# Performance work log

Hardware: AMD Instinct MI355X
Metric: run time of the kernel (lower is better)

The kernel has to match this reference:

```python
import jax, jax.numpy as jnp
import numpy as np

N_MOL, N_ATOM, DEG = 32, 128, 32
N = N_MOL * N_ATOM          # 4096 real atoms (no blanks)
P = N * DEG                 # 131072 pairs
N_SENS = 20
SOFT_MIN, SOFT_MAX, HARD_MAX = 0.7, 5.0, 7.5
N_IN, N_OUT, N_HIST = 2, 3, 3
NF1 = 20                    # hipnn1 n_features
NF0 = 2 * NF1               # hipnn0 n_features (doubled in __init__)
NG = 4 * NF1                # gate logits width of InteractLayer W
N_ATOM_LAYERS = 3
NIN0 = 2 + N_HIST           # one-hot over {1,8} + x_h channels


def setup_inputs():
    rng = np.random.default_rng(0)
    species = 1 + 7 * rng.integers(0, 2, size=(N_MOL, N_ATOM))  # values in {1,8}, all nonblank
    base = np.repeat(np.arange(N), DEG)
    local = base % N_ATOM
    neigh = (local + 1 + rng.integers(0, N_ATOM - 1, size=P)) % N_ATOM  # neighbor != self
    pair_second = (base // N_ATOM) * N_ATOM + neigh                     # same-molecule pairs
    key = jax.random.key(0)
    ks = jax.random.split(key, 20)
    g = lambda i, shape, s=0.1: jax.random.normal(ks[i], shape, dtype=jnp.float32) * s
    return {
        "species": jnp.asarray(species, jnp.int32),
        "coordinates": jax.random.uniform(ks[0], (N_MOL, N_ATOM, 3), jnp.float32, 0.0, 6.0),
        "x_h": g(1, (N_MOL, N_ATOM, N_HIST)),
        "x_raw": g(2, (N_MOL, N_ATOM, N_IN)),
        "pair_first": jnp.asarray(base, jnp.int32),
        "pair_second": jnp.asarray(pair_second, jnp.int32),
        "h0_int_w": g(3, (N_SENS, NIN0, NF0)),
        "h0_self_w": g(4, (NIN0, NF0)),
        "h0_self_b": g(5, (NF0,)),
        "h0_aw": g(6, (N_ATOM_LAYERS, NF0, NF0)),
        "h0_ab": g(7, (N_ATOM_LAYERS, NF0)),
        "h1_int_w": g(8, (N_SENS, 1, NF1)),
        "h1_self_w": g(9, (1, NF1)),
        "h1_self_b": g(10, (NF1,)),
        "h1_aw": g(11, (N_ATOM_LAYERS, NF1, NF1)),
        "h1_ab": g(12, (N_ATOM_LAYERS, NF1)),
        "W_int_w": g(13, (N_SENS, NF0, NG)),
        "W_self_w": g(14, (NF0, NG)),
        "W_self_b": g(15, (NG,)),
        "pw0": g(16, (NIN0, 1)),
        "pw1": g(17, (NF1, 1)),
        "pb1": g(18, (1,)),
    }


def _sensitivity(d):
    # inverse-distance gaussian sensitivities with smooth hard cutoff
    mu = jnp.linspace(1.0 / SOFT_MAX, 1.0 / SOFT_MIN, N_SENS)
    sigma = (1.0 / SOFT_MIN - 1.0 / SOFT_MAX) / N_SENS
    sense = jnp.exp(-0.5 * jnp.square((1.0 / d[:, None] - mu) / sigma))
    cut = jnp.where(d < HARD_MAX, jnp.square(jnp.cos(jnp.pi * d / (2.0 * HARD_MAX))), 0.0)
    return sense * cut[:, None]                                     # (P, n_sens)


def _interact(x, sense, pf, ps, int_w, self_w, self_b):
    # gather neighbor features, weight by sensitivities, scatter-add to center atom
    msg = sense[:, :, None] * x[ps][:, None, :]                     # (P, ns, fin)
    env = jax.ops.segment_sum(msg, pf, num_segments=N)              # (N, ns, fin)
    ns, fin, fout = int_w.shape
    return env.reshape(N, ns * fin) @ int_w.reshape(ns * fin, fout) + x @ self_w + self_b


def _hipnn(x, sense, pf, ps, int_w, self_w, self_b, aw, ab):
    y = jax.nn.softplus(_interact(x, sense, pf, ps, int_w, self_w, self_b))
    for i in range(aw.shape[0]):
        y = jax.nn.softplus(y @ aw[i] + ab[i])
    return x, y   # (input features, final block features)


def _forward(coordinates, x_h, x_raw,
             h0_int_w, h0_self_w, h0_self_b, h0_aw, h0_ab,
             h1_int_w, h1_self_w, h1_self_b, h1_aw, h1_ab,
             W_int_w, W_self_w, W_self_b, pw0, pw1, pb1,
             species, pair_first, pair_second):
    enc = (species.reshape(-1)[:, None] == jnp.array([1, 8])).astype(jnp.float32)  # OneHotSpecies
    coord = coordinates.reshape(-1, 3)
    diff = coord[pair_first] - coord[pair_second]
    d = jnp.sqrt(jnp.sum(diff * diff, axis=-1) + 1e-12)
    sense = _sensitivity(d)
    ind_f = jnp.concatenate([enc, x_h.reshape(N, N_HIST)], axis=1)  # (N, 5)
    f0_in, f0_out = _hipnn(ind_f, sense, pair_first, pair_second,
                           h0_int_w, h0_self_w, h0_self_b, h0_aw, h0_ab)
    c_t, h_t = f0_out[:, : NF0 // 2], f0_out[:, NF0 // 2:]

    def onestep(x_in, h_t, c_t):
        x_t = _hipnn(x_in, sense, pair_first, pair_second,
                     h1_int_w, h1_self_w, h1_self_b, h1_aw, h1_ab)[1]
        tmp = _interact(jnp.concatenate([x_t, h_t], axis=-1), sense,
                        pair_first, pair_second, W_int_w, W_self_w, W_self_b)
        tmp = tmp.reshape(N, NF1, 4)
        o_t = jax.nn.sigmoid(tmp[..., 3])
        c_t = jax.nn.sigmoid(tmp[..., 1]) * c_t + jax.nn.sigmoid(tmp[..., 0]) * jnp.tanh(tmp[..., 2])
        h_t = o_t * jnp.tanh(c_t)
        return o_t, h_t, c_t

    xr = x_raw.reshape(N, N_IN)
    o_t = None
    for t in range(N_IN):
        o_t, h_t, c_t = onestep(xr[:, t:t + 1], h_t, c_t)
    x0 = f0_in @ pw0 + o_t @ pw1 + pb1                              # PredictAtom
    outs = []
    for t in range(N_OUT):
        o_t, h_t, c_t = onestep(x0, h_t, c_t)
        x0 = f0_in @ pw0 + o_t @ pw1 + pb1
        outs.append(x0)
    return jnp.concatenate(outs, axis=-1)                           # (N, n_out)


def reference(species, coordinates, x_h, x_raw, pair_first, pair_second,
              h0_int_w, h0_self_w, h0_self_b, h0_aw, h0_ab,
              h1_int_w, h1_self_w, h1_self_b, h1_aw, h1_ab,
              W_int_w, W_self_w, W_self_b, pw0, pw1, pb1):
    return _forward(coordinates, x_h, x_raw,
                    h0_int_w, h0_self_w, h0_self_b, h0_aw, h0_ab,
                    h1_int_w, h1_self_w, h1_self_b, h1_aw, h1_ab,
                    W_int_w, W_self_w, W_self_b, pw0, pw1, pb1,
                    species, pair_first, pair_second)
```

## Files before the change

kernel.cpp:

```cpp
#include <hip/hip_runtime.h>
#include <hip/hip_bf16.h>


#define DEG 32
#define NA 4096
#define NP 131072

typedef __hip_bfloat16 bf16;
typedef __attribute__((ext_vector_type(8))) short short8v;
typedef __attribute__((ext_vector_type(4))) float f32x4;

#define Z0F 16.27906976744186f
#define DZ  1.0526315789473684f

__device__ __forceinline__ float frcp(float x){ return __builtin_amdgcn_rcpf(x); }
__device__ __forceinline__ float sigmoid_f(float x){ return frcp(1.f + __expf(-x)); }
__device__ __forceinline__ float tanh_f(float x){ return 1.f - 2.f*frcp(__expf(2.f*x)+1.f); }
__device__ __forceinline__ float softplus_f(float x){ return fmaxf(x,0.f) + __logf(1.f + __expf(-fabsf(x))); }
__device__ __forceinline__ unsigned bf16pack(float lo, float hi){
  unsigned ul = __float_as_uint(lo), uh = __float_as_uint(hi);
  unsigned rl = (ul + 0x7fffu + ((ul>>16)&1u)) >> 16;
  unsigned rh = (uh + 0x7fffu + ((uh>>16)&1u)) & 0xffff0000u;
  return rl | rh;
}
__device__ __forceinline__ unsigned short b16u(float v){
  unsigned u = __float_as_uint(v);
  return (unsigned short)((u + 0x7fffu + ((u>>16)&1u)) >> 16);
}
union UU { unsigned u[4]; short8v v; };
union U4 { uint4 q; short8v v; unsigned u[4]; };

__device__ __forceinline__ void wr_tile(unsigned* er, f32x4 D, int M, int N,
                                        int lg, int lr, int l){
  #pragma unroll
  for(int r=0;r<4;r++){
    float vd = D[r];
    float pr = __shfl_xor(vd, 1);
    int s = M*16 + lg*4 + r, f = N*16 + lr;
    if(!(l&1) && s<20 && f<40) er[s*20 + (f>>1)] = bf16pack(vd, pr);
  }
}

__global__ __launch_bounds__(256) void k_prep(
    const int* __restrict__ pf, const int* __restrict__ ps,
    const int* __restrict__ species,
    const float* __restrict__ coord, const float* __restrict__ xh,
    const float* __restrict__ pw0, const float* __restrict__ pb1,
    const float* __restrict__ Wint, const float* __restrict__ Wself,
    unsigned short* __restrict__ svA, unsigned* __restrict__ svB,
    unsigned* __restrict__ Amf,
    bf16* __restrict__ Wmf, float* __restrict__ indf, float* __restrict__ proj0)
{
  int b = blockIdx.x, t = threadIdx.x;
  if (b < 512){
    int p = b*256 + t;
    int i = pf[p], j = ps[p];
    float dx = coord[i*3+0]-coord[j*3+0];
    float dy = coord[i*3+1]-coord[j*3+1];
    float dz = coord[i*3+2]-coord[j*3+2];
    float d = sqrtf(dx*dx+dy*dy+dz*dz + 1e-12f);
    float cu = 0.f;
    if (d < 7.5f){ float c = __cosf(d * 0.20943951023931953f); cu = c*c; }
    float z0 = (1.f/d - 0.2f)*Z0F;
    int atom = p>>5, k = p&31;
    float sv[20], svn[20];
    #pragma unroll
    for(int s=0;s<20;s++){
      float z = z0 - (float)s*DZ;
      sv[s] = cu*__expf(-0.5f*z*z);
    }
    #pragma unroll
    for(int s=0;s<20;s++) svn[s] = __shfl_down(sv[s], 1);
    #pragma unroll
    for(int s=0;s<20;s++) svA[atom*640 + s*32 + k] = b16u(sv[s]);
    #pragma unroll
    for(int s2=0;s2<10;s2++) svB[atom*320 + k*10 + s2] = bf16pack(sv[2*s2], sv[2*s2+1]);
    if (!(k&1)){
      int lg = k>>3, q = (k>>1)&3;
      #pragma unroll
      for(int s=0;s<20;s++){
        int lr = s&15, fr = s>>4;
        Amf[atom*512 + (lg*16+lr)*8 + fr*4 + q] = bf16pack(sv[s], svn[s]);
      }
    } else {
      int idx = k>>1;
      int lg2 = idx>>2, q2 = idx&3;
      #pragma unroll
      for(int j2=0;j2<12;j2++){
        int lr = 4+j2;
        Amf[atom*512 + (lg2*16+lr)*8 + 4 + q2] = 0u;
      }
    }
  } else if (b < 782){
    int tid = (b-512)*256 + t;
    if (tid < 69120){
      int j = tid & 7, l = (tid>>3) & 63, gt = (tid>>9)%5, slab = tid/2560;
      int k = slab*32 + ((l>>4)<<3) + j;
      int g = gt*16 + (l&15);
      float v = 0.f;
      if (k < 800)      v = Wint[k*80+g];
      else if (k < 840) v = Wself[(k-800)*80+g];
      Wmf[tid] = __float2bfloat16(v);
    }
  } else {
    int tid = (b-782)*256 + t;
    if (tid < NA){
      int sp = species[tid];
      float f0 = (sp==1)?1.f:0.f, f1 = (sp==8)?1.f:0.f;
      float f2=xh[tid*3+0], f3=xh[tid*3+1], f4=xh[tid*3+2];
      indf[tid*5+0]=f0; indf[tid*5+1]=f1; indf[tid*5+2]=f2;
      indf[tid*5+3]=f3; indf[tid*5+4]=f4;
      proj0[tid] = pb1[0] + f0*pw0[0] + f1*pw0[1] + f2*pw0[2]
                 + f3*pw0[3] + f4*pw0[4];
    }
  }
}

#define F_SVT  0
#define F_INDF 10432
#define F_ENV0 11072
#define F_Y0A  12672
#define F_Y0B  13312
#define F_NB   13952
#define F_SMEM 14080
__device__ void f0_body(float* smem, int t, int mol, int sib,
    const int* __restrict__ ps, const unsigned* __restrict__ svB,
    const float* __restrict__ indf_g,
    const float* __restrict__ h0_iw, const float* __restrict__ h0_sw,
    const float* __restrict__ h0_sb, const float* __restrict__ h0_aw,
    const float* __restrict__ h0_ab,
    float* __restrict__ c_g, unsigned* __restrict__ h_p)
{
  const int nbase = mol*128;
  const int abase = nbase + sib*16;
  float* svt  = smem + F_SVT;
  float* indf = smem + F_INDF;
  float* env0 = smem + F_ENV0;
  float* y0a  = smem + F_Y0A;
  float* y0b  = smem + F_Y0B;
  unsigned char* nb8 = (unsigned char*)(smem + F_NB);

  for(int i=t;i<5120;i+=512){
    int a=i/320, q=i%320, k=q/10, s2=q%10;
    unsigned v = svB[(abase+a)*320 + q];
    float* dst = svt + a*652 + k*20 + s2*2;
    dst[0] = __uint_as_float(v<<16);
    dst[1] = __uint_as_float(v & 0xffff0000u);
  }
  for(int i=t;i<640;i+=512) indf[i] = indf_g[nbase*5 + i];
  if (t < 512) nb8[t] = (unsigned char)(ps[abase*DEG + t] - nbase);
  __syncthreads();

  for(int task=t; task<1600; task+=512){
    int a = task/100, e = task%100, s = e/5, f = e%5;
    const float* svr = svt + a*652;
    const unsigned char* nbr = nb8 + a*32;
    float acc = 0.f;
    for(int k=0;k<32;k++) acc += svr[k*20+s]*indf[nbr[k]*5+f];
    env0[a*100+e] = acc;
  }
  __syncthreads();
  for(int task=t; task<640; task+=512){
    int a=task/40, o=task%40, row=(sib*16)+a;
    float acc = h0_sb[o];
    #pragma unroll
    for(int f=0;f<5;f++) acc += indf[row*5+f]*h0_sw[f*40+o];
    for(int e=0;e<100;e++) acc += env0[a*100+e]*h0_iw[e*40+o];
    y0a[a*40+o] = softplus_f(acc);
  }
  __syncthreads();
  float* cur = y0a; float* nxt = y0b;
  for(int l=0;l<3;l++){
    for(int task=t; task<640; task+=512){
      int a=task/40, o=task%40;
      float acc = h0_ab[l*40+o];
      for(int f=0;f<40;f++) acc += cur[a*40+f]*h0_aw[l*1600+f*40+o];
      nxt[a*40+o] = softplus_f(acc);
    }
    __syncthreads();
    float* tswap=cur; cur=nxt; nxt=tswap;
  }
  if (t < 320){ int a=t/20,u=t%20; c_g[(abase+a)*20+u] = cur[a*40+u]; }
  if (t < 160){ int a=t/10,p=t%10;
    h_p[NA*10 + (abase+a)*10+p] = bf16pack(cur[a*40+20+2*p], cur[a*40+21+2*p]); }
}

#define X_XIN 0
#define X_NB  128
#define X_WTS 256
#define X_EV1 1956
#define X_YA  2276
#define X_YB  2596
__device__ void xt_body(float* smem, int t, int mol, int sib,
    const int* __restrict__ ps, const unsigned short* __restrict__ svA,
    const float* __restrict__ xraw, const float* __restrict__ x0g,
    int use_raw, int col,
    const float* __restrict__ h1_iw, const float* __restrict__ h1_sw,
    const float* __restrict__ h1_sb, const float* __restrict__ h1_aw,
    const float* __restrict__ h1_ab,
    unsigned* __restrict__ xt_p)
{
  const int nbase = mol*128;
  const int abase = nbase + sib*16;
  float* xin = smem + X_XIN;
  unsigned char* nb8 = (unsigned char*)(smem + X_NB);
  float* wts = smem + X_WTS;
  float* ev1 = smem + X_EV1;
  float* yA  = smem + X_YA;
  float* yB  = smem + X_YB;

  if (t < 128) xin[t] = use_raw ? xraw[(nbase+t)*2+col] : x0g[nbase+t];
  if (t < 512) nb8[t] = (unsigned char)(ps[abase*DEG+t] - nbase);
  for(int i=t;i<1700;i+=512){
    float v;
    if(i<400){ int o=i/20,s=i%20; v=h1_iw[s*20+o]; }
    else if(i<420) v=h1_sw[i-400];
    else if(i<440) v=h1_sb[i-420];
    else if(i<1640){ int q=i-440,L=q/400,rem=q%400,o=rem/20,f=rem%20; v=h1_aw[L*400+f*20+o]; }
    else v=h1_ab[i-1640];
    wts[i]=v;
  }
  __syncthreads();

  if (t < 320){
    int a=t/20, s=t%20;
    const uint4* sp4 = (const uint4*)(svA + (abase+a)*640 + s*32);
    const unsigned char* nbr = nb8 + a*32;
    float acc = 0.f;
    #pragma unroll
    for(int c4=0;c4<4;c4++){
      uint4 w = sp4[c4];
      unsigned wu[4] = {w.x,w.y,w.z,w.w};
      #pragma unroll
      for(int j=0;j<4;j++){
        float flo = __uint_as_float(wu[j]<<16);
        float fhi = __uint_as_float(wu[j] & 0xffff0000u);
        int k = c4*8 + 2*j;
        acc += flo*xin[nbr[k]] + fhi*xin[nbr[k+1]];
      }
    }
    ev1[t] = acc;
  }
  __syncthreads();
  if (t < 320){
    int a=t/20, o=t%20;
    float acc = wts[420+o] + xin[sib*16+a]*wts[400+o];
    const float* e = ev1 + a*20; const float* w = wts + o*20;
    #pragma unroll
    for(int s=0;s<20;s++) acc += e[s]*w[s];
    yA[t] = softplus_f(acc);
  }
  __syncthreads();
  #pragma unroll
  for(int L=0;L<2;L++){
    const float* src = (L==0)? yA : yB;
    float* dst       = (L==0)? yB : yA;
    if (t < 320){
      int a=t/20, o=t%20;
      float acc = wts[1640+L*20+o];
      const float* sr = src + a*20; const float* w = wts + 440 + L*400 + o*20;
      #pragma unroll
      for(int f=0;f<20;f++) acc += sr[f]*w[f];
      dst[t] = softplus_f(acc);
    }
    __syncthreads();
  }
  if (t < 160){
    int a=t/10, p=t%10, o0=2*p, o1=o0+1;
    const float* e = yA + a*20;
    float a0 = wts[1680+o0], a1 = wts[1680+o1];
    const float* wA = wts + 1240 + o0*20;
    const float* wB = wA + 20;
    #pragma unroll
    for(int f=0;f<20;f++){ a0 += e[f]*wA[f]; a1 += e[f]*wB[f]; }
    xt_p[(abase+a)*10+p] = bf16pack(softplus_f(a0), softplus_f(a1));
  }
}

__global__ __launch_bounds__(512) void k_fx(
    const int* __restrict__ ps, const unsigned* __restrict__ svB,
    const unsigned short* __restrict__ svA,
    const float* __restrict__ indf_g, const float* __restrict__ xraw,
    const float* __restrict__ h0_iw, const float* __restrict__ h0_sw,
    const float* __restrict__ h0_sb, const float* __restrict__ h0_aw,
    const float* __restrict__ h0_ab,
    const float* __restrict__ h1_iw, const float* __restrict__ h1_sw,
    const float* __restrict__ h1_sb, const float* __restrict__ h1_aw,
    const float* __restrict__ h1_ab,
    float* __restrict__ c_g, unsigned* __restrict__ h_p,
    unsigned* __restrict__ xt_p0, unsigned* __restrict__ xt_p1)
{
  __shared__ float smem[F_SMEM];
  const int t = threadIdx.x;
  const int sel = blockIdx.x >> 8;
  const int blk = blockIdx.x & 255;
  const int mol = blk & 31, sib = blk >> 5;
  if (sel == 0)
    f0_body(smem, t, mol, sib, ps, svB, indf_g,
            h0_iw,h0_sw,h0_sb,h0_aw,h0_ab, c_g, h_p);
  else
    xt_body(smem, t, mol, sib, ps, svA, xraw, (const float*)0, 1, sel-1,
            h1_iw,h1_sw,h1_sb,h1_aw,h1_ab, (sel==1)? xt_p0 : xt_p1);
}

__global__ __launch_bounds__(512) void k_xt(
    const int* __restrict__ ps, const unsigned short* __restrict__ svA,
    const float* __restrict__ xraw, const float* __restrict__ x0g,
    const float* __restrict__ h1_iw, const float* __restrict__ h1_sw,
    const float* __restrict__ h1_sb, const float* __restrict__ h1_aw,
    const float* __restrict__ h1_ab,
    unsigned* __restrict__ xt_p)
{
  __shared__ float smem[2916];
  const int t = threadIdx.x;
  const int mol = blockIdx.x & 31, sib = blockIdx.x >> 5;
  xt_body(smem, t, mol, sib, ps, svA, xraw, x0g, 0, 0,
          h1_iw,h1_sw,h1_sb,h1_aw,h1_ab, xt_p);
}

#define E_XHP 0
#define E_NB  2688
#define E_PRJ 2752
#define E_PW1 2768
#define E_ER  2792
#define E_TMP (E_ER+6976)
#define E_RED (E_TMP+1280)
#define E_HT  (E_RED+160)
#define E_SMEM (E_HT+160)
__global__ __launch_bounds__(512) void k_env(
    const int* __restrict__ ps, const unsigned* __restrict__ Amf,
    const unsigned* __restrict__ xt_p, const unsigned* __restrict__ h_p,
    int rpar, int wpar,
    const bf16* __restrict__ Wmf, const float* __restrict__ Wb,
    const float* __restrict__ pw1, const float* __restrict__ proj0,
    float* __restrict__ c_g, unsigned* __restrict__ h_po,
    float* __restrict__ x0g, float* __restrict__ outp, int out_col)
{
  __shared__ float smem[E_SMEM];
  const int t = threadIdx.x;
  const int mol = blockIdx.x & 31, sib = blockIdx.x >> 5;
  const int nbase = mol*128;
  const int abase = nbase + sib*8;
  unsigned* xhp = (unsigned*)(smem + E_XHP);
  unsigned char* nb8 = (unsigned char*)(smem + E_NB);
  float* prj  = smem + E_PRJ;
  float* pw1s = smem + E_PW1;
  unsigned* er = (unsigned*)(smem + E_ER);

  for(int i=t;i<1280;i+=512){
    int r=i/10, p=i%10;
    xhp[r*21+p]    = xt_p[(nbase+r)*10+p];
    xhp[r*21+10+p] = h_p[rpar*NA*10 + (nbase+r)*10+p];
  }
  if (t < 256) nb8[t] = (unsigned char)(ps[abase*DEG + t] - nbase);
  if (t < 8)  prj[t] = proj0[abase+t];
  if (t < 20) pw1s[t] = pw1[t];
  __syncthreads();

  {
    const int wv = t>>6, l = t&63, lg = (t>>4)&3, lr = t&15;
    f32x4 z4 = {0.f,0.f,0.f,0.f};
    int a = wv;
    int atom_g = abase + a;
    const U4* ap = (const U4*)(Amf + (unsigned)atom_g*512u + (unsigned)l*8u);
    U4 A0 = ap[0], A1 = ap[1];
    const unsigned* nbw = (const unsigned*)(nb8 + a*32 + lg*8);
    unsigned nw0=nbw[0], nw1=nbw[1];
    int nl[8];
    #pragma unroll
    for(int j2=0;j2<4;j2++){ nl[j2]=(nw0>>(8*j2))&255; nl[4+j2]=(nw1>>(8*j2))&255; }
    f32x4 d00,d01,d02,d10,d11,d12;
    {
      UU B; int f=lr; unsigned sh=(f&1)<<4;
      #pragma unroll
      for(int q=0;q<4;q++){
        unsigned wlo = xhp[nl[2*q]*21 + (f>>1)];
        unsigned whi = xhp[nl[2*q+1]*21 + (f>>1)];
        B.u[q] = ((wlo>>sh)&0xffffu) | (((whi>>sh)&0xffffu)<<16);
      }
      d00=__builtin_amdgcn_mfma_f32_16x16x32_bf16(A0.v,B.v,z4,0,0,0);
      d10=__builtin_amdgcn_mfma_f32_16x16x32_bf16(A1.v,B.v,z4,0,0,0);
    }
    {
      UU B; int f=16+lr; unsigned sh=(f&1)<<4;
      #pragma unroll
      for(int q=0;q<4;q++){
        unsigned wlo = xhp[nl[2*q]*21 + (f>>1)];
        unsigned whi = xhp[nl[2*q+1]*21 + (f>>1)];
        B.u[q] = ((wlo>>sh)&0xffffu) | (((whi>>sh)&0xffffu)<<16);
      }
      d01=__builtin_amdgcn_mfma_f32_16x16x32_bf16(A0.v,B.v,z4,0,0,0);
      d11=__builtin_amdgcn_mfma_f32_16x16x32_bf16(A1.v,B.v,z4,0,0,0);
    }
    {
      UU B; int f=32+lr; unsigned sh=(f&1)<<4; int val=(f<40);
      #pragma unroll
      for(int q=0;q<4;q++){
        if (val){
          unsigned wlo = xhp[nl[2*q]*21 + (f>>1)];
          unsigned whi = xhp[nl[2*q+1]*21 + (f>>1)];
          B.u[q] = ((wlo>>sh)&0xffffu) | (((whi>>sh)&0xffffu)<<16);
        } else B.u[q] = 0u;
      }
      d02=__builtin_amdgcn_mfma_f32_16x16x32_bf16(A0.v,B.v,z4,0,0,0);
      d12=__builtin_amdgcn_mfma_f32_16x16x32_bf16(A1.v,B.v,z4,0,0,0);
    }
    unsigned* era = er + a*436;
    wr_tile(era,d00,0,0,lg,lr,l); wr_tile(era,d01,0,1,lg,lr,l);
    wr_tile(era,d02,0,2,lg,lr,l); wr_tile(era,d10,1,0,lg,lr,l);
    wr_tile(era,d11,1,1,lg,lr,l); wr_tile(era,d12,1,2,lg,lr,l);
  }
  if (t < 160){ int a=t/20, f2=t%20; er[a*436+400+f2] = xhp[(sib*8+a)*21+f2]; }
  if (t < 256) er[(t>>4)*436 + 420 + (t&15)] = 0u;
  __syncthreads();

  float* tmp_s = smem + E_TMP;
  if (t < 320){
    int wv = t >> 6, l = t & 63;
    f32x4 cacc = {0.f,0.f,0.f,0.f};
    const unsigned* abase_p = er + (l & 15)*436 + ((l>>4)<<2);
    const short8v* bptr = (const short8v*)Wmf + (wv*64 + l);
    #pragma unroll 3
    for(int slab=0; slab<27; ++slab){
      short8v av = *(const short8v*)(abase_p + slab*16);
      short8v bv = bptr[slab*320];
      cacc = __builtin_amdgcn_mfma_f32_16x16x32_bf16(av, bv, cacc, 0,0,0);
    }
    int g = wv*16 + (l & 15);
    float wb = Wb[g];
    int r0 = (l>>4)*4;
    #pragma unroll
    for(int r=0;r<4;r++) tmp_s[(r0+r)*80 + g] = cacc[r] + wb;
  }
  __syncthreads();

  float* red = smem + E_RED;
  float* ht  = smem + E_HT;
  if (t < 160){
    int a=t/20, u=t%20;
    float4 tv = *(const float4*)(tmp_s + a*80 + u*4);
    float cold = c_g[(abase+a)*20+u];
    float cnew = sigmoid_f(tv.y)*cold + sigmoid_f(tv.x)*tanh_f(tv.z);
    float og   = sigmoid_f(tv.w);
    c_g[(abase+a)*20+u] = cnew;
    ht[a*20+u]  = og*tanh_f(cnew);
    red[a*20+u] = og*pw1s[u];
  }
  __syncthreads();
  if (t < 80){
    int a=t/10, p=t%10;
    h_po[wpar*NA*10 + (abase+a)*10+p] = bf16pack(ht[a*20+2*p], ht[a*20+2*p+1]);
  }
  if (t < 8){
    float accx = prj[t];
    #pragma unroll
    for(int u=0;u<20;u++) accx += red[t*20+u];
    x0g[abase+t] = accx;
    if (out_col >= 0) outp[(abase+t)*3+out_col] = accx;
  }
}

extern "C" void kernel_launch(void* const* d_in, const int* in_sizes, int n_in,
                              void* d_out, int out_size, void* d_ws, size_t ws_size,
                              hipStream_t stream)
{
  const int*   species = (const int*)  d_in[0];
  const float* coord   = (const float*)d_in[1];
  const float* xh      = (const float*)d_in[2];
  const float* xraw    = (const float*)d_in[3];
  const int*   pf      = (const int*)  d_in[4];
  const int*   ps      = (const int*)  d_in[5];
  const float* h0_intw = (const float*)d_in[6];
  const float* h0_sw   = (const float*)d_in[7];
  const float* h0_sb   = (const float*)d_in[8];
  const float* h0_aw   = (const float*)d_in[9];
  const float* h0_ab   = (const float*)d_in[10];
  const float* h1_intw = (const float*)d_in[11];
  const float* h1_sw   = (const float*)d_in[12];
  const float* h1_sb   = (const float*)d_in[13];
  const float* h1_aw   = (const float*)d_in[14];
  const float* h1_ab   = (const float*)d_in[15];
  const float* W_intw  = (const float*)d_in[16];
  const float* W_sw    = (const float*)d_in[17];
  const float* W_sb    = (const float*)d_in[18];
  const float* pw0     = (const float*)d_in[19];
  const float* pw1     = (const float*)d_in[20];
  const float* pb1     = (const float*)d_in[21];
  float* outp = (float*)d_out;

  float* w = (float*)d_ws;
  unsigned short* svA = (unsigned short*)w;  w += NA*320;
  unsigned* svB = (unsigned*)w;              w += NA*320;
  unsigned* Amf = (unsigned*)w;              w += NA*512;
  bf16* Wmf = (bf16*)w;                      w += 34560;
  float* indf = w;                           w += NA*5;
  float* proj0 = w;                          w += NA;
  unsigned* xt_pA = (unsigned*)w;            w += NA*10;
  unsigned* xt_pB = (unsigned*)w;            w += NA*10;
  unsigned* h_p = (unsigned*)w;              w += 2*NA*10;
  float* x0g = w;                            w += NA;
  float* c_g = w;                            w += NA*20;

  k_prep<<<800,256,0,stream>>>(pf,ps,species,coord,xh,pw0,pb1,W_intw,W_sw,
                               svA,svB,Amf,Wmf,indf,proj0);
  k_fx<<<768,512,0,stream>>>(ps,svB,svA,indf,xraw,
                             h0_intw,h0_sw,h0_sb,h0_aw,h0_ab,
                             h1_intw,h1_sw,h1_sb,h1_aw,h1_ab,
                             c_g,h_p,xt_pA,xt_pB);
  for(int step=0; step<5; ++step){
    int rpar = (step+1)&1, wpar = step&1;
    int out_col = (step>=2)? (step-2) : -1;
    unsigned* xtp = (step&1)? xt_pB : xt_pA;
    if (step >= 2)
      k_xt<<<256,512,0,stream>>>(ps,svA,xraw,x0g,
                                 h1_intw,h1_sw,h1_sb,h1_aw,h1_ab, xtp);
    k_env<<<512,512,0,stream>>>(ps,Amf,xtp,h_p,rpar,wpar,
                                Wmf,W_sb,pw1,proj0,
                                c_g,h_p,x0g,outp,out_col);
  }
}
```

Baseline: 99.34 us.

## Fuse prep and first-step feature kernels by recomputing sensitivities in-block

Merges the prep kernel and the initial hipnn0/x_t kernel into one launch. The hipnn0 and first x_t blocks now recompute distances and Gaussian sensitivities from coordinates in shared memory instead of reading the svB/indf buffers the prep stage wrote. This removes one launch, the inter-kernel dependency, and the svB/indf global writes and reads. In exchange the expf work per pair is done again inside the per-molecule blocks, and those blocks now run concurrently with the prep blocks instead of after them.

```diff
diff --git a/kernel.cpp b/kernel.cpp
--- a/kernel.cpp
+++ b/kernel.cpp
@@ -41,20 +41,58 @@
   }
 }
 
-__global__ __launch_bounds__(256) void k_prep(
-    const int* __restrict__ pf, const int* __restrict__ ps,
-    const int* __restrict__ species,
+__device__ __forceinline__ void stage_ivcu(float2* ivcu, unsigned char* nb8,
+    int t, int abase, int nbase,
+    const int* __restrict__ ps, const float* __restrict__ coord){
+  int pg = abase*DEG + t;
+  int i = abase + (t>>5);
+  int j = ps[pg];
+  float dx = coord[i*3+0]-coord[j*3+0];
+  float dy = coord[i*3+1]-coord[j*3+1];
+  float dz = coord[i*3+2]-coord[j*3+2];
+  float d = sqrtf(dx*dx+dy*dy+dz*dz + 1e-12f);
+  float cu = 0.f;
+  if (d < 7.5f){ float c = __cosf(d * 0.20943951023931953f); cu = c*c; }
+  ivcu[t] = make_float2(1.f/d, cu);
+  nb8[t] = (unsigned char)(j - nbase);
+}
+
+#define I_IVCU 0
+#define I_NB   1024
+#define I_INDF 1152
+#define I_ENV0 1792
+#define I_Y0A  3392
+#define I_Y0B  4032
+#define I_XIN  1152
+#define I_WTS  1280
+#define I_EV1  2980
+#define I_YA   3300
+#define I_YB   3620
+#define I_SMEM 4672
+
+__global__ __launch_bounds__(512) void k_init(
+    const int* __restrict__ ps, const int* __restrict__ species,
     const float* __restrict__ coord, const float* __restrict__ xh,
+    const float* __restrict__ xraw,
     const float* __restrict__ pw0, const float* __restrict__ pb1,
     const float* __restrict__ Wint, const float* __restrict__ Wself,
-    unsigned short* __restrict__ svA, unsigned* __restrict__ svB,
-    unsigned* __restrict__ Amf,
-    bf16* __restrict__ Wmf, float* __restrict__ indf, float* __restrict__ proj0)
+    const float* __restrict__ h0_iw, const float* __restrict__ h0_sw,
+    const float* __restrict__ h0_sb, const float* __restrict__ h0_aw,
+    const float* __restrict__ h0_ab,
+    const float* __restrict__ h1_iw, const float* __restrict__ h1_sw,
+    const float* __restrict__ h1_sb, const float* __restrict__ h1_aw,
+    const float* __restrict__ h1_ab,
+    unsigned short* __restrict__ svA, unsigned* __restrict__ Amf,
+    bf16* __restrict__ Wmf, float* __restrict__ proj0,
+    float* __restrict__ c_g, unsigned* __restrict__ h_p,
+    unsigned* __restrict__ xt_p0, unsigned* __restrict__ xt_p1)
 {
-  int b = blockIdx.x, t = threadIdx.x;
-  if (b < 512){
-    int p = b*256 + t;
-    int i = pf[p], j = ps[p];
+  __shared__ float smem[I_SMEM];
+  const int b = blockIdx.x, t = threadIdx.x;
+
+  if (b < 256){
+    int p = b*512 + t;
+    int i = p>>5, j = ps[p];
     float dx = coord[i*3+0]-coord[j*3+0];
     float dy = coord[i*3+1]-coord[j*3+1];
     float dz = coord[i*3+2]-coord[j*3+2];
@@ -73,8 +111,6 @@
     for(int s=0;s<20;s++) svn[s] = __shfl_down(sv[s], 1);
     #pragma unroll
     for(int s=0;s<20;s++) svA[atom*640 + s*32 + k] = b16u(sv[s]);
-    #pragma unroll
-    for(int s2=0;s2<10;s2++) svB[atom*320 + k*10 + s2] = bf16pack(sv[2*s2], sv[2*s2+1]);
     if (!(k&1)){
       int lg = k>>3, q = (k>>1)&3;
       #pragma unroll
@@ -91,98 +127,161 @@
         Amf[atom*512 + (lg2*16+lr)*8 + 4 + q2] = 0u;
       }
     }
-  } else if (b < 782){
-    int tid = (b-512)*256 + t;
-    if (tid < 69120){
-      int j = tid & 7, l = (tid>>3) & 63, gt = (tid>>9)%5, slab = tid/2560;
-      int k = slab*32 + ((l>>4)<<3) + j;
-      int g = gt*16 + (l&15);
-      float v = 0.f;
-      if (k < 800)      v = Wint[k*80+g];
-      else if (k < 840) v = Wself[(k-800)*80+g];
-      Wmf[tid] = __float2bfloat16(v);
-    }
-  } else {
-    int tid = (b-782)*256 + t;
+    return;
+  }
+  if (b < 391){
+    int tid = (b-256)*512 + t;
+    int j = tid & 7, l = (tid>>3) & 63, gt = (tid>>9)%5, slab = tid/2560;
+    int k = slab*32 + ((l>>4)<<3) + j;
+    int g = gt*16 + (l&15);
+    float v = 0.f;
+    if (k < 800)      v = Wint[k*80+g];
+    else if (k < 840) v = Wself[(k-800)*80+g];
+    Wmf[tid] = __float2bfloat16(v);
+    return;
+  }
+  if (b < 399){
+    int tid = (b-391)*512 + t;
     if (tid < NA){
       int sp = species[tid];
       float f0 = (sp==1)?1.f:0.f, f1 = (sp==8)?1.f:0.f;
-      float f2=xh[tid*3+0], f3=xh[tid*3+1], f4=xh[tid*3+2];
-      indf[tid*5+0]=f0; indf[tid*5+1]=f1; indf[tid*5+2]=f2;
-      indf[tid*5+3]=f3; indf[tid*5+4]=f4;
-      proj0[tid] = pb1[0] + f0*pw0[0] + f1*pw0[1] + f2*pw0[2]
-                 + f3*pw0[3] + f4*pw0[4];
-    }
-  }
-}
-
-#define F_SVT  0
-#define F_INDF 10432
-#define F_ENV0 11072
-#define F_Y0A  12672
-#define F_Y0B  13312
-#define F_NB   13952
-#define F_SMEM 14080
-__device__ void f0_body(float* smem, int t, int mol, int sib,
-    const int* __restrict__ ps, const unsigned* __restrict__ svB,
-    const float* __restrict__ indf_g,
-    const float* __restrict__ h0_iw, const float* __restrict__ h0_sw,
-    const float* __restrict__ h0_sb, const float* __restrict__ h0_aw,
-    const float* __restrict__ h0_ab,
-    float* __restrict__ c_g, unsigned* __restrict__ h_p)
-{
-  const int nbase = mol*128;
-  const int abase = nbase + sib*16;
-  float* svt  = smem + F_SVT;
-  float* indf = smem + F_INDF;
-  float* env0 = smem + F_ENV0;
-  float* y0a  = smem + F_Y0A;
-  float* y0b  = smem + F_Y0B;
-  unsigned char* nb8 = (unsigned char*)(smem + F_NB);
-
-  for(int i=t;i<5120;i+=512){
-    int a=i/320, q=i%320, k=q/10, s2=q%10;
-    unsigned v = svB[(abase+a)*320 + q];
-    float* dst = svt + a*652 + k*20 + s2*2;
-    dst[0] = __uint_as_float(v<<16);
-    dst[1] = __uint_as_float(v & 0xffff0000u);
-  }
-  for(int i=t;i<640;i+=512) indf[i] = indf_g[nbase*5 + i];
-  if (t < 512) nb8[t] = (unsigned char)(ps[abase*DEG + t] - nbase);
-  __syncthreads();
-
-  for(int task=t; task<1600; task+=512){
-    int a = task/100, e = task%100, s = e/5, f = e%5;
-    const float* svr = svt + a*652;
-    const unsigned char* nbr = nb8 + a*32;
-    float acc = 0.f;
-    for(int k=0;k<32;k++) acc += svr[k*20+s]*indf[nbr[k]*5+f];
-    env0[a*100+e] = acc;
-  }
-  __syncthreads();
-  for(int task=t; task<640; task+=512){
-    int a=task/40, o=task%40, row=(sib*16)+a;
-    float acc = h0_sb[o];
-    #pragma unroll
-    for(int f=0;f<5;f++) acc += indf[row*5+f]*h0_sw[f*40+o];
-    for(int e=0;e<100;e++) acc += env0[a*100+e]*h0_iw[e*40+o];
-    y0a[a*40+o] = softplus_f(acc);
-  }
-  __syncthreads();
-  float* cur = y0a; float* nxt = y0b;
-  for(int l=0;l<3;l++){
+      proj0[tid] = pb1[0] + f0*pw0[0] + f1*pw0[1] + xh[tid*3+0]*pw0[2]
+                 + xh[tid*3+1]*pw0[3] + xh[tid*3+2]*pw0[4];
+    }
+    return;
+  }
+
+  float2* ivcu = (float2*)(smem + I_IVCU);
+  unsigned char* nb8 = (unsigned char*)(smem + I_NB);
+
+  if (b < 655){
+    int blk = b - 399;
+    int mol = blk & 31, sib = blk >> 5;
+    int nbase = mol*128, abase = nbase + sib*16;
+    float* indf = smem + I_INDF;
+    float* env0 = smem + I_ENV0;
+    float* y0a  = smem + I_Y0A;
+    float* y0b  = smem + I_Y0B;
+    stage_ivcu(ivcu, nb8, t, abase, nbase, ps, coord);
+    if (t < 128){
+      int sp = species[nbase+t];
+      indf[t*5+0] = (sp==1)?1.f:0.f;
+      indf[t*5+1] = (sp==8)?1.f:0.f;
+      indf[t*5+2] = xh[(nbase+t)*3+0];
+      indf[t*5+3] = xh[(nbase+t)*3+1];
+      indf[t*5+4] = xh[(nbase+t)*3+2];
+    }
+    __syncthreads();
+    for(int task=t; task<1600; task+=512){
+      int a = task/100, e = task%100, s = e/5, f = e%5;
+      const float2* ivr = ivcu + a*32;
+      const unsigned char* nbr = nb8 + a*32;
+      float sz = (float)s*DZ, acc = 0.f;
+      for(int k=0;k<32;k++){
+        float2 vc = ivr[k];
+        float z = (vc.x-0.2f)*Z0F - sz;
+        acc += vc.y*__expf(-0.5f*z*z)*indf[nbr[k]*5+f];
+      }
+      env0[a*100+e] = acc;
+    }
+    __syncthreads();
     for(int task=t; task<640; task+=512){
-      int a=task/40, o=task%40;
-      float acc = h0_ab[l*40+o];
-      for(int f=0;f<40;f++) acc += cur[a*40+f]*h0_aw[l*1600+f*40+o];
-      nxt[a*40+o] = softplus_f(acc);
-    }
-    __syncthreads();
-    float* tswap=cur; cur=nxt; nxt=tswap;
-  }
-  if (t < 320){ int a=t/20,u=t%20; c_g[(abase+a)*20+u] = cur[a*40+u]; }
-  if (t < 160){ int a=t/10,p=t%10;
-    h_p[NA*10 + (abase+a)*10+p] = bf16pack(cur[a*40+20+2*p], cur[a*40+21+2*p]); }
+      int a=task/40, o=task%40, row=(sib*16)+a;
+      float acc = h0_sb[o];
+      #pragma unroll
+      for(int f=0;f<5;f++) acc += indf[row*5+f]*h0_sw[f*40+o];
+      for(int e=0;e<100;e++) acc += env0[a*100+e]*h0_iw[e*40+o];
+      y0a[a*40+o] = softplus_f(acc);
+    }
+    __syncthreads();
+    float* cur = y0a; float* nxt = y0b;
+    for(int l=0;l<3;l++){
+      for(int task=t; task<640; task+=512){
+        int a=task/40, o=task%40;
+        float acc = h0_ab[l*40+o];
+        for(int f=0;f<40;f++) acc += cur[a*40+f]*h0_aw[l*1600+f*40+o];
+        nxt[a*40+o] = softplus_f(acc);
+      }
+      __syncthreads();
+      float* tswap=cur; cur=nxt; nxt=tswap;
+    }
+    if (t < 320){ int a=t/20,u=t%20; c_g[(abase+a)*20+u] = cur[a*40+u]; }
+    if (t < 160){ int a=t/10,p=t%10;
+      h_p[NA*10 + (abase+a)*10+p] = bf16pack(cur[a*40+20+2*p], cur[a*40+21+2*p]); }
+    return;
+  }
+
+  {
+    int sel = (b < 911) ? 0 : 1;
+    int blk = b - (sel ? 911 : 655);
+    int mol = blk & 31, sib = blk >> 5;
+    int nbase = mol*128, abase = nbase + sib*16;
+    float* xin = smem + I_XIN;
+    float* wts = smem + I_WTS;
+    float* ev1 = smem + I_EV1;
+    float* yA  = smem + I_YA;
+    float* yB  = smem + I_YB;
+    unsigned* xt_p = sel ? xt_p1 : xt_p0;
+
+    stage_ivcu(ivcu, nb8, t, abase, nbase, ps, coord);
+    if (t < 128) xin[t] = xraw[(nbase+t)*2+sel];
+    for(int i=t;i<1700;i+=512){
+      float v;
+      if(i<400){ int o=i/20,s=i%20; v=h1_iw[s*20+o]; }
+      else if(i<420) v=h1_sw[i-400];
+      else if(i<440) v=h1_sb[i-420];
+      else if(i<1640){ int q=i-440,L=q/400,rem=q%400,o=rem/20,f=rem%20; v=h1_aw[L*400+f*20+o]; }
+      else v=h1_ab[i-1640];
+      wts[i]=v;
+    }
+    __syncthreads();
+    if (t < 320){
+      int a=t/20, s=t%20;
+      const float2* ivr = ivcu + a*32;
+      const unsigned char* nbr = nb8 + a*32;
+      float sz=(float)s*DZ, acc=0.f;
+      for(int k=0;k<32;k++){
+        float2 vc = ivr[k];
+        float z = (vc.x-0.2f)*Z0F - sz;
+        acc += vc.y*__expf(-0.5f*z*z)*xin[nbr[k]];
+      }
+      ev1[t] = acc;
+    }
+    __syncthreads();
+    if (t < 320){
+      int a=t/20, o=t%20;
+      float acc = wts[420+o] + xin[sib*16+a]*wts[400+o];
+      const float* e = ev1 + a*20; const float* w = wts + o*20;
+      #pragma unroll
+      for(int s=0;s<20;s++) acc += e[s]*w[s];
+      yA[t] = softplus_f(acc);
+    }
+    __syncthreads();
+    #pragma unroll
+    for(int L=0;L<2;L++){
+      const float* src = (L==0)? yA : yB;
+      float* dst       = (L==0)? yB : yA;
+      if (t < 320){
+        int a=t/20, o=t%20;
+        float acc = wts[1640+L*20+o];
+        const float* sr = src + a*20; const float* w = wts + 440 + L*400 + o*20;
+        #pragma unroll
+        for(int f=0;f<20;f++) acc += sr[f]*w[f];
+        dst[t] = softplus_f(acc);
+      }
+      __syncthreads();
+    }
+    if (t < 160){
+      int a=t/10, p=t%10, o0=2*p, o1=o0+1;
+      const float* e = yA + a*20;
+      float a0 = wts[1680+o0], a1 = wts[1680+o1];
+      const float* wA = wts + 1240 + o0*20;
+      const float* wB = wA + 20;
+      #pragma unroll
+      for(int f=0;f<20;f++){ a0 += e[f]*wA[f]; a1 += e[f]*wB[f]; }
+      xt_p[(abase+a)*10+p] = bf16pack(softplus_f(a0), softplus_f(a1));
+    }
+  }
 }
 
 #define X_XIN 0
@@ -191,15 +290,17 @@
 #define X_EV1 1956
 #define X_YA  2276
 #define X_YB  2596
-__device__ void xt_body(float* smem, int t, int mol, int sib,
+__global__ __launch_bounds__(512) void k_xt(
     const int* __restrict__ ps, const unsigned short* __restrict__ svA,
-    const float* __restrict__ xraw, const float* __restrict__ x0g,
-    int use_raw, int col,
+    const float* __restrict__ x0g,
     const float* __restrict__ h1_iw, const float* __restrict__ h1_sw,
     const float* __restrict__ h1_sb, const float* __restrict__ h1_aw,
     const float* __restrict__ h1_ab,
     unsigned* __restrict__ xt_p)
 {
+  __shared__ float smem[2916];
+  const int t = threadIdx.x;
+  const int mol = blockIdx.x & 31, sib = blockIdx.x >> 5;
   const int nbase = mol*128;
   const int abase = nbase + sib*16;
   float* xin = smem + X_XIN;
@@ -209,8 +310,8 @@
   float* yA  = smem + X_YA;
   float* yB  = smem + X_YB;
 
-  if (t < 128) xin[t] = use_raw ? xraw[(nbase+t)*2+col] : x0g[nbase+t];
-  if (t < 512) nb8[t] = (unsigned char)(ps[abase*DEG+t] - nbase);
+  if (t < 128) xin[t] = x0g[nbase+t];
+  nb8[t] = (unsigned char)(ps[abase*DEG+t] - nbase);
   for(int i=t;i<1700;i+=512){
     float v;
     if(i<400){ int o=i/20,s=i%20; v=h1_iw[s*20+o]; }
@@ -275,47 +376,6 @@
     for(int f=0;f<20;f++){ a0 += e[f]*wA[f]; a1 += e[f]*wB[f]; }
     xt_p[(abase+a)*10+p] = bf16pack(softplus_f(a0), softplus_f(a1));
   }
-}
-
-__global__ __launch_bounds__(512) void k_fx(
-    const int* __restrict__ ps, const unsigned* __restrict__ svB,
-    const unsigned short* __restrict__ svA,
-    const float* __restrict__ indf_g, const float* __restrict__ xraw,
-    const float* __restrict__ h0_iw, const float* __restrict__ h0_sw,
-    const float* __restrict__ h0_sb, const float* __restrict__ h0_aw,
-    const float* __restrict__ h0_ab,
-    const float* __restrict__ h1_iw, const float* __restrict__ h1_sw,
-    const float* __restrict__ h1_sb, const float* __restrict__ h1_aw,
-    const float* __restrict__ h1_ab,
-    float* __restrict__ c_g, unsigned* __restrict__ h_p,
-    unsigned* __restrict__ xt_p0, unsigned* __restrict__ xt_p1)
-{
-  __shared__ float smem[F_SMEM];
-  const int t = threadIdx.x;
-  const int sel = blockIdx.x >> 8;
-  const int blk = blockIdx.x & 255;
-  const int mol = blk & 31, sib = blk >> 5;
-  if (sel == 0)
-    f0_body(smem, t, mol, sib, ps, svB, indf_g,
-            h0_iw,h0_sw,h0_sb,h0_aw,h0_ab, c_g, h_p);
-  else
-    xt_body(smem, t, mol, sib, ps, svA, xraw, (const float*)0, 1, sel-1,
-            h1_iw,h1_sw,h1_sb,h1_aw,h1_ab, (sel==1)? xt_p0 : xt_p1);
-}
-
-__global__ __launch_bounds__(512) void k_xt(
-    const int* __restrict__ ps, const unsigned short* __restrict__ svA,
-    const float* __restrict__ xraw, const float* __restrict__ x0g,
-    const float* __restrict__ h1_iw, const float* __restrict__ h1_sw,
-    const float* __restrict__ h1_sb, const float* __restrict__ h1_aw,
-    const float* __restrict__ h1_ab,
-    unsigned* __restrict__ xt_p)
-{
-  __shared__ float smem[2916];
-  const int t = threadIdx.x;
-  const int mol = blockIdx.x & 31, sib = blockIdx.x >> 5;
-  xt_body(smem, t, mol, sib, ps, svA, xraw, x0g, 0, 0,
-          h1_iw,h1_sw,h1_sb,h1_aw,h1_ab, xt_p);
 }
 
 #define E_XHP 0
@@ -487,13 +547,12 @@
   const float* pw1     = (const float*)d_in[20];
   const float* pb1     = (const float*)d_in[21];
   float* outp = (float*)d_out;
+  (void)pf;
 
   float* w = (float*)d_ws;
   unsigned short* svA = (unsigned short*)w;  w += NA*320;
-  unsigned* svB = (unsigned*)w;              w += NA*320;
   unsigned* Amf = (unsigned*)w;              w += NA*512;
   bf16* Wmf = (bf16*)w;                      w += 34560;
-  float* indf = w;                           w += NA*5;
   float* proj0 = w;                          w += NA;
   unsigned* xt_pA = (unsigned*)w;            w += NA*10;
   unsigned* xt_pB = (unsigned*)w;            w += NA*10;
@@ -501,18 +560,16 @@
   float* x0g = w;                            w += NA;
   float* c_g = w;                            w += NA*20;
 
-  k_prep<<<800,256,0,stream>>>(pf,ps,species,coord,xh,pw0,pb1,W_intw,W_sw,
-                               svA,svB,Amf,Wmf,indf,proj0);
-  k_fx<<<768,512,0,stream>>>(ps,svB,svA,indf,xraw,
-                             h0_intw,h0_sw,h0_sb,h0_aw,h0_ab,
-                             h1_intw,h1_sw,h1_sb,h1_aw,h1_ab,
-                             c_g,h_p,xt_pA,xt_pB);
+  k_init<<<1167,512,0,stream>>>(ps,species,coord,xh,xraw,pw0,pb1,W_intw,W_sw,
+                                h0_intw,h0_sw,h0_sb,h0_aw,h0_ab,
+                                h1_intw,h1_sw,h1_sb,h1_aw,h1_ab,
+                                svA,Amf,Wmf,proj0,c_g,h_p,xt_pA,xt_pB);
   for(int step=0; step<5; ++step){
     int rpar = (step+1)&1, wpar = step&1;
     int out_col = (step>=2)? (step-2) : -1;
     unsigned* xtp = (step&1)? xt_pB : xt_pA;
     if (step >= 2)
-      k_xt<<<256,512,0,stream>>>(ps,svA,xraw,x0g,
+      k_xt<<<256,512,0,stream>>>(ps,svA,x0g,
                                  h1_intw,h1_sw,h1_sb,h1_aw,h1_ab, xtp);
     k_env<<<512,512,0,stream>>>(ps,Amf,xtp,h_p,rpar,wpar,
                                 Wmf,W_sb,pw1,proj0,
```

New measurement: 89.97 us (median of 2 runs). 9.4% less time.
